# Performance work log

Hardware: AMD Instinct MI355X
Metric: run time of the kernel (lower is better)

Reference implementation:

```python
import jax, jax.numpy as jnp
import numpy as np
import math

DIM = 1536
NH = 12
HD = 128          # head_dim
C = HD // 2       # 64 complex rope dims
MAX_ATTN = 15 * 880
EPS = 1e-6


def _rope_tables(max_len=1024, d=HD, theta=10000.0):
    # Wan rope_params: freqs = cat([rope(1024, d-4*(d//6)), rope(1024, 2*(d//6)), rope(1024, 2*(d//6))], dim=1)
    d0 = d - 4 * (d // 6)   # 44 -> 22 complex dims (F axis)
    d1 = 2 * (d // 6)       # 42 -> 21 complex dims (H and W axes)
    parts = []
    for dd in (d0, d1, d1):
        inv = 1.0 / theta ** (np.arange(0, dd, 2, dtype=np.float32) / dd)
        parts.append(np.outer(np.arange(max_len, dtype=np.float32), inv))
    ang = np.concatenate(parts, axis=1)                 # [1024, C]
    return np.stack([np.cos(ang), np.sin(ang)], -1)     # [1024, C, 2]


def rmsnorm(x, g, eps=EPS):
    return x * jax.lax.rsqrt(jnp.mean(x * x, axis=-1, keepdims=True) + eps) * g


def rope_apply(xq, f, h, w, freqs, start_frame):
    # xq: [B, S, N, D]; freqs: [1024, C, 2] cos/sin tables; S = f*h*w
    b, s, n, d = xq.shape
    c = d // 2
    s0 = c - 2 * (c // 3)   # F-axis complex dims (22)
    s1 = c // 3             # H/W-axis complex dims (21)
    cos, sin = freqs[..., 0], freqs[..., 1]

    def per_token(tab):
        tf = jnp.broadcast_to(tab[start_frame:start_frame + f, :s0][:, None, None, :], (f, h, w, s0))
        th = jnp.broadcast_to(tab[:h, s0:s0 + s1][None, :, None, :], (f, h, w, s1))
        tw = jnp.broadcast_to(tab[:w, s0 + s1:][None, None, :, :], (f, h, w, s1))
        return jnp.concatenate([tf, th, tw], -1).reshape(1, s, 1, c)

    pc, ps = per_token(cos), per_token(sin)
    xr = xq.reshape(b, s, n, c, 2)
    re, im = xr[..., 0], xr[..., 1]
    out = jnp.stack([re * pc - im * ps, re * ps + im * pc], -1)
    return out.reshape(b, s, n, d)


def _forward(x, wq, bq, wk, bk, wv, bv, wo, bo, gq, gk, freqs, k_cache, v_cache, f, h, w, current_start):
    b, s, _ = x.shape
    frame_seqlen = h * w
    start_frame = current_start // frame_seqlen

    q = rmsnorm(x @ wq.T + bq, gq).reshape(b, s, NH, HD)
    k = rmsnorm(x @ wk.T + bk, gk).reshape(b, s, NH, HD)
    v = (x @ wv.T + bv).reshape(b, s, NH, HD)

    rq = rope_apply(q, f, h, w, freqs, start_frame)
    rk = rope_apply(k, f, h, w, freqs, start_frame)

    current_end = current_start + s
    # cache not full: append new keys/values at [current_start:current_end]
    k_cache = jax.lax.dynamic_update_slice(k_cache, rk, (0, current_start, 0, 0))
    v_cache = jax.lax.dynamic_update_slice(v_cache, v, (0, current_start, 0, 0))

    win_start = max(0, current_end - MAX_ATTN)
    kk = k_cache[:, win_start:current_end]   # [B, Lk, N, D]
    vv = v_cache[:, win_start:current_end]

    scale = 1.0 / math.sqrt(HD)
    scores = jnp.einsum('bqnd,bknd->bnqk', rq, kk) * scale
    attn = jax.nn.softmax(scores, axis=-1)
    out = jnp.einsum('bnqk,bknd->bqnd', attn, vv).reshape(b, s, DIM)
    return out @ wo.T + bo


def setup_inputs() -> dict:
    key = jax.random.key(0)
    ks = jax.random.split(key, 8)
    B, S, CACHE = 1, 880, 18 * 880
    x = jax.random.normal(ks[0], (B, S, DIM), jnp.float32)

    def lin(k):
        k1, k2 = jax.random.split(k)
        wgt = jax.random.normal(k1, (DIM, DIM), jnp.float32) / math.sqrt(DIM)
        bia = jax.random.normal(k2, (DIM,), jnp.float32) * 0.01
        return wgt, bia

    wq, bq = lin(ks[1]); wk, bk = lin(ks[2]); wv, bv = lin(ks[3]); wo, bo = lin(ks[4])
    gq = jnp.ones((DIM,), jnp.float32)
    gk = jnp.ones((DIM,), jnp.float32)
    freqs = jnp.asarray(_rope_tables())
    k_cache = jax.random.normal(ks[5], (B, CACHE, NH, HD), jnp.float32) * 0.5
    v_cache = jax.random.normal(ks[6], (B, CACHE, NH, HD), jnp.float32) * 0.5
    grid_sizes = jnp.array([1, 22, 40], jnp.int32)  # (F, H, W), H*W = 880
    return dict(x=x, wq=wq, bq=bq, wk=wk, bk=bk, wv=wv, bv=bv, wo=wo, bo=bo,
                gq=gq, gk=gk, freqs=freqs, k_cache=k_cache, v_cache=v_cache,
                grid_sizes=grid_sizes, current_start=10560)


def reference(x, wq, bq, wk, bk, wv, bv, wo, bo, gq, gk, freqs, k_cache, v_cache, grid_sizes, current_start):
    f, h, w = (int(grid_sizes[0]), int(grid_sizes[1]), int(grid_sizes[2]))
    return _forward(x, wq, bq, wk, bk, wv, bv, wo, bo, gq, gk, freqs,
                    k_cache, v_cache, f, h, w, int(current_start))
```

## Files before the change

kernel.cpp:

```cpp
#include <hip/hip_runtime.h>

#define NHEADS 12
#define HDIM 128
#define MODEL_DIM 1536
#define MAX_ATTN_W 13200
#define NSPLIT 18

typedef unsigned short u16;
typedef unsigned int u32;
typedef float f32x4 __attribute__((ext_vector_type(4)));
typedef float f32x16 __attribute__((ext_vector_type(16)));
typedef __bf16 bf16x8 __attribute__((ext_vector_type(8)));

static __device__ __forceinline__ u16 f2bf(float f) {
  union { __bf16 h; u16 u; } cv;
  cv.h = (__bf16)f;
  return cv.u;
}
static __device__ __forceinline__ float bf2f(u16 u) {
  union { u32 u; float f; } cv;
  cv.u = ((u32)u) << 16;
  return cv.f;
}
static __device__ __forceinline__ u32 pk2(float a, float b) {
  return (u32)f2bf(a) | ((u32)f2bf(b) << 16);
}
static __device__ __forceinline__ void gload_lds16(const void* g, void* l) {
  __builtin_amdgcn_global_load_lds(
      (const __attribute__((address_space(1))) unsigned int*)g,
      (__attribute__((address_space(3))) unsigned int*)l, 16, 0, 0);
}

__global__ void k_conv_bf16(const float* __restrict__ src, u16* __restrict__ dst, int n4) {
  int i = blockIdx.x * blockDim.x + threadIdx.x;
  if (i >= n4) return;
  float4 v = ((const float4*)src)[i];
  ((uint2*)dst)[i] = make_uint2(pk2(v.x, v.y), pk2(v.z, v.w));
}

__global__ void k_conv_bf16_w4(const float* __restrict__ s0, const float* __restrict__ s1,
                               const float* __restrict__ s2, const float* __restrict__ s3,
                               u16* __restrict__ d0, u16* __restrict__ d1,
                               u16* __restrict__ d2, u16* __restrict__ d3, int n4) {
  int i = blockIdx.x * blockDim.x + threadIdx.x;
  if (i >= n4) return;
  const int which = blockIdx.y;
  const float* src = (which == 0) ? s0 : (which == 1) ? s1 : (which == 2) ? s2 : s3;
  u16* dst = (which == 0) ? d0 : (which == 1) ? d1 : (which == 2) ? d2 : d3;
  float4 v = ((const float4*)src)[i];
  ((uint2*)dst)[i] = make_uint2(pk2(v.x, v.y), pk2(v.z, v.w));
}

__global__ void k_build_kold(const float* __restrict__ kc, u16* __restrict__ K_all,
                             const int* __restrict__ csp, int S, int KVcap) {
  const int cs = csp[0];
  const int ce = cs + S;
  int wst = ce - MAX_ATTN_W; if (wst < 0) wst = 0;
  const int oldlen = cs - wst;
  const long per = (long)oldlen * 16;
  const long total = per * NHEADS;
  for (long c = blockIdx.x * (long)blockDim.x + threadIdx.x; c < total;
       c += (long)gridDim.x * blockDim.x) {
    int n = (int)(c / per);
    long r = c - (long)n * per;
    int jo = (int)(r >> 4);
    int dc = ((int)r & 15) * 8;
    const float* s = kc + ((size_t)(wst + jo) * NHEADS + n) * HDIM + dc;
    float4 a = *(const float4*)s;
    float4 b = *(const float4*)(s + 4);
    uint4 o;
    o.x = pk2(a.x, a.y);
    o.y = pk2(a.z, a.w);
    o.z = pk2(b.x, b.y);
    o.w = pk2(b.z, b.w);
    *(uint4*)(K_all + ((size_t)n * KVcap + jo) * HDIM + dc) = o;
  }
}

__launch_bounds__(256)
__global__ void k_build_vtold(const float* __restrict__ vc, u16* __restrict__ VT,
                              const int* __restrict__ csp, int S, int KVcap) {
  __shared__ u16 tile[64][130];
  const int cs = csp[0];
  const int ce = cs + S;
  int wst = ce - MAX_ATTN_W; if (wst < 0) wst = 0;
  const int oldlen = cs - wst;
  const int n = blockIdx.y;
  const int j0 = blockIdx.x * 64;
  if (j0 >= oldlen) return;
  const int tid = threadIdx.x;

  #pragma unroll
  for (int i = 0; i < 8; i++) {
    int idx = tid + 256 * i;
    int j = idx >> 5;
    int dc = (idx & 31) * 4;
    float4 v = make_float4(0.f, 0.f, 0.f, 0.f);
    if (j0 + j < oldlen)
      v = *(const float4*)(vc + ((size_t)(wst + j0 + j) * NHEADS + n) * HDIM + dc);
    *(u32*)&tile[j][dc] = pk2(v.x, v.y);
    *(u32*)&tile[j][dc + 2] = pk2(v.z, v.w);
  }
  __syncthreads();

  const int d = tid >> 1;
  const int jh = (tid & 1) * 32;
  alignas(16) u16 buf[32];
  #pragma unroll
  for (int j = 0; j < 32; j++) buf[j] = tile[jh + j][d];
  u16* dst = VT + ((size_t)n * HDIM + d) * KVcap + j0 + jh;
  if (j0 + jh + 32 <= oldlen) {
    #pragma unroll
    for (int c = 0; c < 4; c++)
      *(uint4*)(dst + c * 8) = *(const uint4*)&buf[c * 8];
  } else {
    for (int j = 0; j < 32 && j0 + jh + j < oldlen; j++) dst[j] = buf[j];
  }
}

__launch_bounds__(256)
__global__ void k_gemm_o128(const u16* __restrict__ A, const u16* __restrict__ B,
                            const float* __restrict__ bias, float* __restrict__ out,
                            int M, int N, int K) {
  __shared__ __align__(16) u16 Al[128][40];
  __shared__ __align__(16) u16 Bl[128][40];
  const int n0 = blockIdx.y * 128;
  const int tid = threadIdx.x;
  const int wid = tid >> 6, l = tid & 63, l31 = l & 31, hi = l >> 5;
  const int wr = wid >> 1, wc = wid & 1;
  const int m0 = blockIdx.x * 128;
  f32x16 acc[2][2];
  #pragma unroll
  for (int mt = 0; mt < 2; mt++)
    #pragma unroll
    for (int nt = 0; nt < 2; nt++)
      #pragma unroll
      for (int j = 0; j < 16; j++) acc[mt][nt][j] = 0.f;
  const int row = tid >> 2, colc = (tid & 3) * 8;
  for (int k0 = 0; k0 < K; k0 += 32) {
    __syncthreads();
    uint4 a0 = *(const uint4*)(A + (size_t)(m0 + row) * K + k0 + colc);
    uint4 a1 = *(const uint4*)(A + (size_t)(m0 + row + 64) * K + k0 + colc);
    uint4 b0 = *(const uint4*)(B + (size_t)(n0 + row) * K + k0 + colc);
    uint4 b1 = *(const uint4*)(B + (size_t)(n0 + row + 64) * K + k0 + colc);
    *(uint4*)&Al[row][colc] = a0;
    *(uint4*)&Al[row + 64][colc] = a1;
    *(uint4*)&Bl[row][colc] = b0;
    *(uint4*)&Bl[row + 64][colc] = b1;
    __syncthreads();
    #pragma unroll
    for (int ks = 0; ks < 2; ks++) {
      bf16x8 af[2], bfr[2];
      #pragma unroll
      for (int mt = 0; mt < 2; mt++)
        af[mt] = *(const bf16x8*)&Al[wr * 64 + mt * 32 + l31][ks * 16 + hi * 8];
      #pragma unroll
      for (int nt = 0; nt < 2; nt++)
        bfr[nt] = *(const bf16x8*)&Bl[wc * 64 + nt * 32 + l31][ks * 16 + hi * 8];
      #pragma unroll
      for (int mt = 0; mt < 2; mt++)
        #pragma unroll
        for (int nt = 0; nt < 2; nt++)
          acc[mt][nt] = __builtin_amdgcn_mfma_f32_32x32x16_bf16(af[mt], bfr[nt], acc[mt][nt], 0, 0, 0);
    }
  }
  #pragma unroll
  for (int mt = 0; mt < 2; mt++)
    #pragma unroll
    for (int nt = 0; nt < 2; nt++) {
      const int col = n0 + wc * 64 + nt * 32 + l31;
      const float bb = bias[col];
      #pragma unroll
      for (int r = 0; r < 16; r++) {
        int rowo = m0 + wr * 64 + mt * 32 + (r & 3) + 8 * (r >> 2) + 4 * hi;
        if (rowo < M) out[(size_t)rowo * N + col] = acc[mt][nt][r] + bb;
      }
    }
}

__launch_bounds__(256)
__global__ void k_gemm_qkv128(const u16* __restrict__ A,
                              const u16* __restrict__ B0, const u16* __restrict__ B1,
                              const u16* __restrict__ B2,
                              const float* __restrict__ bias0, const float* __restrict__ bias1,
                              const float* __restrict__ bias2,
                              float* __restrict__ o0, float* __restrict__ o1, float* __restrict__ o2,
                              int M, int N, int K) {
  __shared__ __align__(16) u16 Al[128][40];
  __shared__ __align__(16) u16 Bl[128][40];
  const int nblk = N / 128;
  const int which = blockIdx.y / nblk;
  const int n0 = (blockIdx.y % nblk) * 128;
  const u16* B = (which == 0) ? B0 : ((which == 1) ? B1 : B2);
  const float* bias = (which == 0) ? bias0 : ((which == 1) ? bias1 : bias2);
  float* out = (which == 0) ? o0 : ((which == 1) ? o1 : o2);
  const int tid = threadIdx.x;
  const int wid = tid >> 6, l = tid & 63, l31 = l & 31, hi = l >> 5;
  const int wr = wid >> 1, wc = wid & 1;
  const int m0 = blockIdx.x * 128;
  f32x16 acc[2][2];
  #pragma unroll
  for (int mt = 0; mt < 2; mt++)
    #pragma unroll
    for (int nt = 0; nt < 2; nt++)
      #pragma unroll
      for (int j = 0; j < 16; j++) acc[mt][nt][j] = 0.f;
  const int row = tid >> 2, colc = (tid & 3) * 8;
  for (int k0 = 0; k0 < K; k0 += 32) {
    __syncthreads();
    uint4 a0 = *(const uint4*)(A + (size_t)(m0 + row) * K + k0 + colc);
    uint4 a1 = *(const uint4*)(A + (size_t)(m0 + row + 64) * K + k0 + colc);
    uint4 b0 = *(const uint4*)(B + (size_t)(n0 + row) * K + k0 + colc);
    uint4 b1 = *(const uint4*)(B + (size_t)(n0 + row + 64) * K + k0 + colc);
    *(uint4*)&Al[row][colc] = a0;
    *(uint4*)&Al[row + 64][colc] = a1;
    *(uint4*)&Bl[row][colc] = b0;
    *(uint4*)&Bl[row + 64][colc] = b1;
    __syncthreads();
    #pragma unroll
    for (int ks = 0; ks < 2; ks++) {
      bf16x8 af[2], bfr[2];
      #pragma unroll
      for (int mt = 0; mt < 2; mt++)
        af[mt] = *(const bf16x8*)&Al[wr * 64 + mt * 32 + l31][ks * 16 + hi * 8];
      #pragma unroll
      for (int nt = 0; nt < 2; nt++)
        bfr[nt] = *(const bf16x8*)&Bl[wc * 64 + nt * 32 + l31][ks * 16 + hi * 8];
      #pragma unroll
      for (int mt = 0; mt < 2; mt++)
        #pragma unroll
        for (int nt = 0; nt < 2; nt++)
          acc[mt][nt] = __builtin_amdgcn_mfma_f32_32x32x16_bf16(af[mt], bfr[nt], acc[mt][nt], 0, 0, 0);
    }
  }
  #pragma unroll
  for (int mt = 0; mt < 2; mt++)
    #pragma unroll
    for (int nt = 0; nt < 2; nt++) {
      const int col = n0 + wc * 64 + nt * 32 + l31;
      const float bb = bias[col];
      #pragma unroll
      for (int r = 0; r < 16; r++) {
        int rowo = m0 + wr * 64 + mt * 32 + (r & 3) + 8 * (r >> 2) + 4 * hi;
        if (rowo < M) out[(size_t)rowo * N + col] = acc[mt][nt][r] + bb;
      }
    }
}

__launch_bounds__(256)
__global__ void k_norm_rope(const float* __restrict__ qp, const float* __restrict__ kp,
                            const float* __restrict__ vp, const float* __restrict__ gq,
                            const float* __restrict__ gk, const float* __restrict__ freqs,
                            const int* __restrict__ gs, const int* __restrict__ csp,
                            int S, int KVcap,
                            u16* __restrict__ rq, u16* __restrict__ K_all,
                            u16* __restrict__ VT) {
  const int t = blockIdx.x;
  const int tid = threadIdx.x;
  const float* q = qp + (size_t)t * MODEL_DIM;
  const float* k = kp + (size_t)t * MODEL_DIM;
  const float* v = vp + (size_t)t * MODEL_DIM;
  float sq = 0.f, sk = 0.f;
  for (int j = tid; j < MODEL_DIM; j += 256) {
    float a = q[j]; sq += a * a;
    float b = k[j]; sk += b * b;
  }
  #pragma unroll
  for (int off = 32; off > 0; off >>= 1) {
    sq += __shfl_down(sq, off, 64);
    sk += __shfl_down(sk, off, 64);
  }
  __shared__ float red[8];
  int wv_ = tid >> 6, l = tid & 63;
  if (l == 0) { red[wv_] = sq; red[4 + wv_] = sk; }
  __syncthreads();
  sq = red[0] + red[1] + red[2] + red[3];
  sk = red[4] + red[5] + red[6] + red[7];
  const float rq_s = rsqrtf(sq * (1.0f / MODEL_DIM) + 1e-6f) * 0.12751744f;
  const float rk_s = rsqrtf(sk * (1.0f / MODEL_DIM) + 1e-6f);

  const int cs = csp[0];
  const int h = gs[1], ww = gs[2];
  const int hw = h * ww;
  const int sf = cs / hw;
  const int fi = t / hw;
  const int rr = t - fi * hw;
  const int hi = rr / ww;
  const int wi = rr - hi * ww;
  const int ce = cs + S;
  int wst = ce - MAX_ATTN_W; if (wst < 0) wst = 0;
  const int jj = cs + t - wst;

  for (int p = tid; p < NHEADS * 64; p += 256) {
    int n = p >> 6, c = p & 63;
    int pos = (c < 22) ? (sf + fi) : ((c < 43) ? hi : wi);
    float cv = freqs[(pos * 64 + c) * 2];
    float sv = freqs[(pos * 64 + c) * 2 + 1];
    int j0 = n * HDIM + 2 * c;
    float qr = q[j0] * rq_s * gq[j0];
    float qi = q[j0 + 1] * rq_s * gq[j0 + 1];
    *(u32*)(rq + ((size_t)n * S + t) * HDIM + 2 * c) = pk2(qr * cv - qi * sv, qr * sv + qi * cv);
    float kr = k[j0] * rk_s * gk[j0];
    float ki = k[j0 + 1] * rk_s * gk[j0 + 1];
    *(u32*)(K_all + ((size_t)n * KVcap + jj) * HDIM + 2 * c) = pk2(kr * cv - ki * sv, kr * sv + ki * cv);
  }
  for (int j = tid; j < MODEL_DIM; j += 256) {
    int n = j >> 7, d = j & 127;
    VT[((size_t)n * HDIM + d) * KVcap + jj] = f2bf(v[j]);
  }
}

__launch_bounds__(256, 3)
__global__ void k_attn_split(const u16* __restrict__ rq, const u16* __restrict__ K_all,
                             const u16* __restrict__ VT,
                             u16* __restrict__ po, float* __restrict__ pm, float* __restrict__ pl,
                             const int* __restrict__ csp, int S, int KVcap, int nqb) {
  __shared__ __align__(16) u16 Klds[64][128];
  __shared__ __align__(16) u16 Vlds[128][64];

  const int tid = threadIdx.x;
  const int wid = tid >> 6;
  const int l = tid & 63;
  const int l31 = l & 31;
  const int hi = l >> 5;
  const int swz = (l31 & 7) << 3;

  const int bx = blockIdx.x;
  const int xcd = bx & 7;
  const int j = bx >> 3;
  const int cl = j / nqb;
  const int qb = j - cl * nqb;
  const int chunkid = cl * 8 + xcd;
  const int head = chunkid / NSPLIT;
  const int split = chunkid - head * NSPLIT;
  const int q0 = qb * 128;

  const int cs = csp[0];
  const int ce = cs + S;
  int wst = ce - MAX_ATTN_W; if (wst < 0) wst = 0;
  const int KV = ce - wst;
  const int chunk = (((KV + NSPLIT - 1) / NSPLIT) + 63) & ~63;
  const int kstart = split * chunk;
  int kend = kstart + chunk; if (kend > KV) kend = KV;

  const size_t pbase = ((size_t)head * NSPLIT + split) * S;
  const int qrow = q0 + wid * 32 + l31;

  if (kstart >= kend) {
    if (qrow < S && hi == 0) { pm[pbase + qrow] = -3.0e38f; pl[pbase + qrow] = 0.f; }
    return;
  }

  bf16x8 qf[8];
  if (qrow < S) {
    const u16* qp = rq + ((size_t)head * S + qrow) * HDIM;
    #pragma unroll
    for (int ds = 0; ds < 8; ds++) qf[ds] = *(const bf16x8*)(qp + ds * 16 + hi * 8);
  } else {
    #pragma unroll
    for (int ds = 0; ds < 8; ds++)
      #pragma unroll
      for (int i = 0; i < 8; i++) qf[ds][i] = (__bf16)0.0f;
  }

  f32x16 o[4];
  #pragma unroll
  for (int dt = 0; dt < 4; dt++)
    #pragma unroll
    for (int j2 = 0; j2 < 16; j2++) o[dt][j2] = 0.f;
  float m_ = -3.0e38f, lsum_ = 0.f;

  const u16* Kh = K_all + (size_t)head * KVcap * HDIM;
  const u16* Vh = VT + (size_t)head * HDIM * KVcap;

  int krow_i[4], kcol_i[4], vd_i[4], vcol_i[4];
  #pragma unroll
  for (int i = 0; i < 4; i++) {
    int kr_ = (wid * 4 + i) * 4 + (l >> 4);
    krow_i[i] = kr_;
    kcol_i[i] = (((l & 15) ^ (kr_ & 7)) << 3);
    int vd_ = (wid * 4 + i) * 8 + (l >> 3);
    vd_i[i] = vd_;
    vcol_i[i] = (((l & 7) ^ (vd_ & 7)) << 3);
  }
  u16* kldst[4];
  u16* vldst[4];
  #pragma unroll
  for (int i = 0; i < 4; i++) {
    kldst[i] = &Klds[0][0] + (wid * 4 + i) * 512;
    vldst[i] = &Vlds[0][0] + (wid * 4 + i) * 512;
  }

  const int ntiles = (kend - kstart + 63) >> 6;

  for (int t = 0; t < ntiles; t++) {
    const int key0 = kstart + (t << 6);
    __syncthreads();
    #pragma unroll
    for (int i = 0; i < 4; i++)
      gload_lds16(Kh + (size_t)(key0 + krow_i[i]) * HDIM + kcol_i[i], kldst[i]);
    #pragma unroll
    for (int i = 0; i < 4; i++)
      gload_lds16(Vh + (size_t)vd_i[i] * KVcap + key0 + vcol_i[i], vldst[i]);
    __syncthreads();

    f32x16 s[2];
    __builtin_amdgcn_s_setprio(1);
    #pragma unroll
    for (int kt = 0; kt < 2; kt++) {
      #pragma unroll
      for (int j2 = 0; j2 < 16; j2++) s[kt][j2] = 0.f;
      #pragma unroll
      for (int ds = 0; ds < 8; ds++) {
        bf16x8 kf = *(const bf16x8*)&Klds[kt * 32 + l31][(ds * 16 + hi * 8) ^ swz];
        s[kt] = __builtin_amdgcn_mfma_f32_32x32x16_bf16(kf, qf[ds], s[kt], 0, 0, 0);
      }
    }
    __builtin_amdgcn_s_setprio(0);

    float tm = -3.0e38f;
    if (key0 + 64 <= kend) {
      #pragma unroll
      for (int kt = 0; kt < 2; kt++)
        #pragma unroll
        for (int r = 0; r < 16; r++) tm = fmaxf(tm, s[kt][r]);
    } else {
      #pragma unroll
      for (int kt = 0; kt < 2; kt++) {
        const int rem = kend - key0 - kt * 32;
        #pragma unroll
        for (int r = 0; r < 16; r++) {
          const int off = (r & 3) + 8 * (r >> 2) + 4 * hi;
          float v = (off < rem) ? s[kt][r] : -3.0e38f;
          s[kt][r] = v;
          tm = fmaxf(tm, v);
        }
      }
    }
    tm = fmaxf(tm, __shfl_xor(tm, 32, 64));

    if (!__all(tm <= m_ + 8.0f)) {
      float nm = fmaxf(m_, tm);
      float alpha = exp2f(m_ - nm);
      m_ = nm;
      lsum_ *= alpha;
      #pragma unroll
      for (int dt = 0; dt < 4; dt++)
        #pragma unroll
        for (int j2 = 0; j2 < 16; j2++) o[dt][j2] *= alpha;
    }

    float rs = 0.f;
    u32 w[2][8];
    #pragma unroll
    for (int kt = 0; kt < 2; kt++)
      #pragma unroll
      for (int j2 = 0; j2 < 8; j2++) {
        float p0 = exp2f(s[kt][2 * j2] - m_);
        float p1 = exp2f(s[kt][2 * j2 + 1] - m_);
        rs += p0 + p1;
        w[kt][j2] = pk2(p0, p1);
      }
    rs += __shfl_xor(rs, 32, 64);
    lsum_ += rs;

    union { u32 u[4]; bf16x8 v; } pf[2][2];
    #pragma unroll
    for (int kt = 0; kt < 2; kt++) {
      u32 xw[8];
      #pragma unroll
      for (int j2 = 0; j2 < 8; j2++) xw[j2] = __shfl_xor(w[kt][j2], 32, 64);
      pf[kt][0].u[0] = hi ? xw[2]    : w[kt][0];
      pf[kt][0].u[1] = hi ? xw[3]    : w[kt][1];
      pf[kt][0].u[2] = hi ? w[kt][2] : xw[0];
      pf[kt][0].u[3] = hi ? w[kt][3] : xw[1];
      pf[kt][1].u[0] = hi ? xw[6]    : w[kt][4];
      pf[kt][1].u[1] = hi ? xw[7]    : w[kt][5];
      pf[kt][1].u[2] = hi ? w[kt][6] : xw[4];
      pf[kt][1].u[3] = hi ? w[kt][7] : xw[5];
    }

    __builtin_amdgcn_s_setprio(1);
    #pragma unroll
    for (int dt = 0; dt < 4; dt++) {
      #pragma unroll
      for (int kt = 0; kt < 2; kt++)
        #pragma unroll
        for (int mm = 0; mm < 2; mm++) {
          bf16x8 vf = *(const bf16x8*)&Vlds[dt * 32 + l31][(kt * 32 + mm * 16 + hi * 8) ^ swz];
          o[dt] = __builtin_amdgcn_mfma_f32_32x32x16_bf16(vf, pf[kt][mm].v, o[dt], 0, 0, 0);
        }
    }
    __builtin_amdgcn_s_setprio(0);
  }

  if (qrow < S) {
    float rl = (lsum_ > 0.f) ? (1.0f / lsum_) : 0.f;
    u16* dst = po + (pbase + qrow) * HDIM;
    #pragma unroll
    for (int dt = 0; dt < 4; dt++)
      #pragma unroll
      for (int jj = 0; jj < 4; jj++) {
        u32 w0 = pk2(o[dt][4 * jj] * rl, o[dt][4 * jj + 1] * rl);
        u32 w1 = pk2(o[dt][4 * jj + 2] * rl, o[dt][4 * jj + 3] * rl);
        *(uint2*)(dst + dt * 32 + 8 * jj + 4 * hi) = make_uint2(w0, w1);
      }
    if (hi == 0) { pm[pbase + qrow] = m_; pl[pbase + qrow] = lsum_; }
  }
}

__global__ void k_attn_reduce(const u16* __restrict__ po, const float* __restrict__ pm,
                              const float* __restrict__ pl, u16* __restrict__ attn_out,
                              int S) {
  const int t = blockIdx.x;
  const int h = blockIdx.y;
  const int d = threadIdx.x;
  float ms[NSPLIT];
  float M = -3.0e38f;
  #pragma unroll
  for (int s = 0; s < NSPLIT; s++) {
    ms[s] = pm[((size_t)h * NSPLIT + s) * S + t];
    M = fmaxf(M, ms[s]);
  }
  float L = 0.f, acc = 0.f;
  #pragma unroll
  for (int s = 0; s < NSPLIT; s++) {
    float wgt = exp2f(ms[s] - M) * pl[((size_t)h * NSPLIT + s) * S + t];
    L += wgt;
    acc += wgt * bf2f(po[(((size_t)h * NSPLIT + s) * S + t) * HDIM + d]);
  }
  attn_out[(size_t)t * MODEL_DIM + h * HDIM + d] = f2bf(acc / L);
}

extern "C" void kernel_launch(void* const* d_in, const int* in_sizes, int n_in,
                              void* d_out, int out_size, void* d_ws, size_t ws_size,
                              hipStream_t stream) {
  (void)n_in; (void)out_size; (void)ws_size;
  const float* x  = (const float*)d_in[0];
  const float* wq = (const float*)d_in[1];
  const float* bq = (const float*)d_in[2];
  const float* wk = (const float*)d_in[3];
  const float* bk = (const float*)d_in[4];
  const float* wv = (const float*)d_in[5];
  const float* bv = (const float*)d_in[6];
  const float* wo = (const float*)d_in[7];
  const float* bo = (const float*)d_in[8];
  const float* gq = (const float*)d_in[9];
  const float* gk = (const float*)d_in[10];
  const float* freqs = (const float*)d_in[11];
  const float* k_cache = (const float*)d_in[12];
  const float* v_cache = (const float*)d_in[13];
  const int* gs  = (const int*)d_in[14];
  const int* csp = (const int*)d_in[15];

  const int S = in_sizes[0] / MODEL_DIM;
  const int CACHE = in_sizes[12] / (NHEADS * HDIM);
  const int KVcap = (CACHE < MAX_ATTN_W) ? CACHE : MAX_ATTN_W;
  const int Mpad = (S + 127) & ~127;
  const int NQB = Mpad / 128;

  char* ws = (char*)d_ws;
  size_t off = 0;
  auto alloc = [&](size_t bytes) {
    char* p = ws + off;
    off += (bytes + 255) & ~(size_t)255;
    return p;
  };
  u16* xb   = (u16*)alloc((size_t)Mpad * MODEL_DIM * 2);
  u16* wqb  = (u16*)alloc((size_t)MODEL_DIM * MODEL_DIM * 2);
  u16* wkb  = (u16*)alloc((size_t)MODEL_DIM * MODEL_DIM * 2);
  u16* wvb  = (u16*)alloc((size_t)MODEL_DIM * MODEL_DIM * 2);
  u16* wob  = (u16*)alloc((size_t)MODEL_DIM * MODEL_DIM * 2);
  float* q_pre = (float*)alloc((size_t)S * MODEL_DIM * 4);
  float* k_pre = (float*)alloc((size_t)S * MODEL_DIM * 4);
  float* v_pre = (float*)alloc((size_t)S * MODEL_DIM * 4);
  u16* rqb   = (u16*)alloc((size_t)NHEADS * S * HDIM * 2);
  u16* K_all = (u16*)alloc((size_t)NHEADS * KVcap * HDIM * 2);
  u16* VT    = (u16*)alloc((size_t)NHEADS * HDIM * KVcap * 2);
  u16* attn_o = (u16*)alloc((size_t)Mpad * MODEL_DIM * 2);
  u16* po    = (u16*)alloc((size_t)NHEADS * NSPLIT * S * HDIM * 2);
  float* pm  = (float*)alloc((size_t)NHEADS * NSPLIT * S * 4);
  float* pl  = (float*)alloc((size_t)NHEADS * NSPLIT * S * 4);

  const int nx4 = S * MODEL_DIM / 4;
  const int nw4 = MODEL_DIM * MODEL_DIM / 4;
  hipLaunchKernelGGL(k_conv_bf16, dim3((nx4 + 255) / 256), dim3(256), 0, stream, x, xb, nx4);
  hipLaunchKernelGGL(k_conv_bf16_w4, dim3((nw4 + 255) / 256, 4), dim3(256), 0, stream,
                     wq, wk, wv, wo, wqb, wkb, wvb, wob, nw4);

  hipLaunchKernelGGL(k_build_kold, dim3(2048), dim3(256), 0, stream, k_cache, K_all, csp, S, KVcap);
  hipLaunchKernelGGL(k_build_vtold, dim3((KVcap + 63) / 64, NHEADS), dim3(256), 0, stream,
                     v_cache, VT, csp, S, KVcap);

  hipLaunchKernelGGL(k_gemm_qkv128, dim3(Mpad / 128, 3 * MODEL_DIM / 128), dim3(256), 0, stream,
                     xb, wqb, wkb, wvb, bq, bk, bv, q_pre, k_pre, v_pre, S, MODEL_DIM, MODEL_DIM);

  hipLaunchKernelGGL(k_norm_rope, dim3(S), dim3(256), 0, stream,
                     q_pre, k_pre, v_pre, gq, gk, freqs, gs, csp, S, KVcap, rqb, K_all, VT);

  hipLaunchKernelGGL(k_attn_split, dim3(NQB * NHEADS * NSPLIT), dim3(256), 0, stream,
                     rqb, K_all, VT, po, pm, pl, csp, S, KVcap, NQB);

  hipLaunchKernelGGL(k_attn_reduce, dim3(S, NHEADS), dim3(128), 0, stream, po, pm, pl, attn_o, S);

  hipLaunchKernelGGL(k_gemm_o128, dim3(Mpad / 128, MODEL_DIM / 128), dim3(256), 0, stream,
                     attn_o, wob, bo, (float*)d_out, S, MODEL_DIM, MODEL_DIM);
}
```

Measured before the change: 312.9 us.

## Replace LDS-staged attention tiles with single-wave blocks loading K/V directly

The split-KV attention kernel moves from 256-thread blocks that stage K and V tiles in shared memory, shared across four waves each handling 32 query rows, to 64-thread single-wave blocks that read K and V fragments straight from global memory. This drops the LDS staging, the two barriers per tile, and the setprio hints, and launches four times as many blocks with 32 queries each. The cost is that K/V reuse across query waves now depends on L2/L1 hits rather than LDS. Global loads are uncoalesced per-lane 16-byte reads, so memory traffic and latency exposure may rise.

After: 380.6 us. 21.6% more time.

```diff
diff --git a/kernel.cpp b/kernel.cpp
--- a/kernel.cpp
+++ b/kernel.cpp
@@ -24,11 +24,6 @@
 }
 static __device__ __forceinline__ u32 pk2(float a, float b) {
   return (u32)f2bf(a) | ((u32)f2bf(b) << 16);
-}
-static __device__ __forceinline__ void gload_lds16(const void* g, void* l) {
-  __builtin_amdgcn_global_load_lds(
-      (const __attribute__((address_space(1))) unsigned int*)g,
-      (__attribute__((address_space(3))) unsigned int*)l, 16, 0, 0);
 }
 
 __global__ void k_conv_bf16(const float* __restrict__ src, u16* __restrict__ dst, int n4) {
@@ -310,20 +305,14 @@
   }
 }
 
-__launch_bounds__(256, 3)
+__launch_bounds__(64)
 __global__ void k_attn_split(const u16* __restrict__ rq, const u16* __restrict__ K_all,
                              const u16* __restrict__ VT,
                              u16* __restrict__ po, float* __restrict__ pm, float* __restrict__ pl,
                              const int* __restrict__ csp, int S, int KVcap, int nqb) {
-  __shared__ __align__(16) u16 Klds[64][128];
-  __shared__ __align__(16) u16 Vlds[128][64];
-
-  const int tid = threadIdx.x;
-  const int wid = tid >> 6;
-  const int l = tid & 63;
+  const int l = threadIdx.x;
   const int l31 = l & 31;
   const int hi = l >> 5;
-  const int swz = (l31 & 7) << 3;
 
   const int bx = blockIdx.x;
   const int xcd = bx & 7;
@@ -333,7 +322,7 @@
   const int chunkid = cl * 8 + xcd;
   const int head = chunkid / NSPLIT;
   const int split = chunkid - head * NSPLIT;
-  const int q0 = qb * 128;
+  const int q0 = qb * 32;
 
   const int cs = csp[0];
   const int ce = cs + S;
@@ -344,7 +333,7 @@
   int kend = kstart + chunk; if (kend > KV) kend = KV;
 
   const size_t pbase = ((size_t)head * NSPLIT + split) * S;
-  const int qrow = q0 + wid * 32 + l31;
+  const int qrow = q0 + l31;
 
   if (kstart >= kend) {
     if (qrow < S && hi == 0) { pm[pbase + qrow] = -3.0e38f; pl[pbase + qrow] = 0.f; }
@@ -373,50 +362,23 @@
   const u16* Kh = K_all + (size_t)head * KVcap * HDIM;
   const u16* Vh = VT + (size_t)head * HDIM * KVcap;
 
-  int krow_i[4], kcol_i[4], vd_i[4], vcol_i[4];
-  #pragma unroll
-  for (int i = 0; i < 4; i++) {
-    int kr_ = (wid * 4 + i) * 4 + (l >> 4);
-    krow_i[i] = kr_;
-    kcol_i[i] = (((l & 15) ^ (kr_ & 7)) << 3);
-    int vd_ = (wid * 4 + i) * 8 + (l >> 3);
-    vd_i[i] = vd_;
-    vcol_i[i] = (((l & 7) ^ (vd_ & 7)) << 3);
-  }
-  u16* kldst[4];
-  u16* vldst[4];
-  #pragma unroll
-  for (int i = 0; i < 4; i++) {
-    kldst[i] = &Klds[0][0] + (wid * 4 + i) * 512;
-    vldst[i] = &Vlds[0][0] + (wid * 4 + i) * 512;
-  }
-
   const int ntiles = (kend - kstart + 63) >> 6;
 
   for (int t = 0; t < ntiles; t++) {
     const int key0 = kstart + (t << 6);
-    __syncthreads();
-    #pragma unroll
-    for (int i = 0; i < 4; i++)
-      gload_lds16(Kh + (size_t)(key0 + krow_i[i]) * HDIM + kcol_i[i], kldst[i]);
-    #pragma unroll
-    for (int i = 0; i < 4; i++)
-      gload_lds16(Vh + (size_t)vd_i[i] * KVcap + key0 + vcol_i[i], vldst[i]);
-    __syncthreads();
 
     f32x16 s[2];
-    __builtin_amdgcn_s_setprio(1);
     #pragma unroll
     for (int kt = 0; kt < 2; kt++) {
+      const u16* krow = Kh + (size_t)(key0 + kt * 32 + l31) * HDIM + hi * 8;
       #pragma unroll
       for (int j2 = 0; j2 < 16; j2++) s[kt][j2] = 0.f;
       #pragma unroll
       for (int ds = 0; ds < 8; ds++) {
-        bf16x8 kf = *(const bf16x8*)&Klds[kt * 32 + l31][(ds * 16 + hi * 8) ^ swz];
+        bf16x8 kf = *(const bf16x8*)(krow + ds * 16);
         s[kt] = __builtin_amdgcn_mfma_f32_32x32x16_bf16(kf, qf[ds], s[kt], 0, 0, 0);
       }
     }
-    __builtin_amdgcn_s_setprio(0);
 
     float tm = -3.0e38f;
     if (key0 + 64 <= kend) {
@@ -480,18 +442,17 @@
       pf[kt][1].u[3] = hi ? w[kt][7] : xw[5];
     }
 
-    __builtin_amdgcn_s_setprio(1);
     #pragma unroll
     for (int dt = 0; dt < 4; dt++) {
+      const u16* vrow = Vh + (size_t)(dt * 32 + l31) * KVcap + key0 + hi * 8;
       #pragma unroll
       for (int kt = 0; kt < 2; kt++)
         #pragma unroll
         for (int mm = 0; mm < 2; mm++) {
-          bf16x8 vf = *(const bf16x8*)&Vlds[dt * 32 + l31][(kt * 32 + mm * 16 + hi * 8) ^ swz];
+          bf16x8 vf = *(const bf16x8*)(vrow + kt * 32 + mm * 16);
           o[dt] = __builtin_amdgcn_mfma_f32_32x32x16_bf16(vf, pf[kt][mm].v, o[dt], 0, 0, 0);
         }
     }
-    __builtin_amdgcn_s_setprio(0);
   }
 
   if (qrow < S) {
@@ -557,7 +518,7 @@
   const int CACHE = in_sizes[12] / (NHEADS * HDIM);
   const int KVcap = (CACHE < MAX_ATTN_W) ? CACHE : MAX_ATTN_W;
   const int Mpad = (S + 127) & ~127;
-  const int NQB = Mpad / 128;
+  const int NQB32 = (S + 31) / 32;
 
   char* ws = (char*)d_ws;
   size_t off = 0;
@@ -598,8 +559,8 @@
   hipLaunchKernelGGL(k_norm_rope, dim3(S), dim3(256), 0, stream,
                      q_pre, k_pre, v_pre, gq, gk, freqs, gs, csp, S, KVcap, rqb, K_all, VT);
 
-  hipLaunchKernelGGL(k_attn_split, dim3(NQB * NHEADS * NSPLIT), dim3(256), 0, stream,
-                     rqb, K_all, VT, po, pm, pl, csp, S, KVcap, NQB);
+  hipLaunchKernelGGL(k_attn_split, dim3(NQB32 * NHEADS * NSPLIT), dim3(64), 0, stream,
+                     rqb, K_all, VT, po, pm, pl, csp, S, KVcap, NQB32);
 
   hipLaunchKernelGGL(k_attn_reduce, dim3(S, NHEADS), dim3(128), 0, stream, po, pm, pl, attn_o, S);
 
```
